# Performance work log

Measured on AMD Instinct MI355X. Metric: run time of the kernel, lower is better.

The kernel has to match this reference:

```python
import jax, jax.numpy as jnp
import numpy as np

B, C, H, N, K = 512, 256, 1024, 500000, 5

_PARAM_DIMS = [("w_in", C, H), ("w_h1", H, H), ("w_s2", H, H), ("w_s3", H, H),
               ("w_h2", H, H), ("w_s1o", H, H), ("w_s2o", H, H), ("w_h3", H, H),
               ("w_mu", H, C), ("w_s", H, C)]


def setup_inputs() -> dict:
    key = jax.random.key(0)
    inp = {}
    k_codes, k_book, k_params = jax.random.split(key, 3)
    inp["codes"] = jax.random.normal(k_codes, (B, C), dtype=jnp.float32)
    inp["codebook"] = jax.random.normal(k_book, (N, C), dtype=jnp.float32)
    ks = jax.random.split(k_params, len(_PARAM_DIMS))
    for (name, fin, fout), k in zip(_PARAM_DIMS, ks):
        k1, k2 = jax.random.split(k)
        s = 1.0 / np.sqrt(fin)
        inp[name] = jax.random.uniform(k1, (fout, fin), minval=-s, maxval=s, dtype=jnp.float32)
        inp["b" + name[1:]] = jax.random.uniform(k2, (fout,), minval=-s, maxval=s, dtype=jnp.float32)
    return inp


def _linear(x, w, b):
    # torch nn.Linear: x @ W^T + b, W is [out, in]
    return x @ w.T + b


def _encode(prev, w_in, b_in, w_h1, b_h1, w_s2, b_s2, w_s3, b_s3,
            w_h2, b_h2, w_s1o, b_s1o, w_s2o, b_s2o, w_h3, b_h3,
            w_mu, b_mu, w_s, b_s):
    i = jnp.tanh(_linear(prev, w_in, b_in))
    h1 = jnp.tanh(_linear(i, w_h1, b_h1))
    s2 = jnp.tanh(_linear(h1, w_s2, b_s2))
    s3 = jnp.tanh(_linear(h1, w_s3, b_s3))
    h2 = jnp.tanh(_linear(h1 + s2, w_h2, b_h2))
    o1 = jnp.tanh(_linear(h1, w_s1o, b_s1o))
    o2 = jnp.tanh(_linear(h2, w_s2o, b_s2o))
    o3 = jnp.tanh(_linear(h2 + s3, w_h3, b_h3))
    out = o1 + o2 + o3
    return _linear(out, w_mu, b_mu), _linear(out, w_s, b_s)


def reference(codes, codebook, w_in, b_in, w_h1, b_h1, w_s2, b_s2, w_s3, b_s3,
              w_h2, b_h2, w_s1o, b_s1o, w_s2o, b_s2o, w_h3, b_h3,
              w_mu, b_mu, w_s, b_s):
    # flat k-NN search: squared L2 dists via the matmul expansion
    codes2 = jnp.sum(codebook * codebook, axis=1)                      # [N]
    dists = (-2.0 * (codes @ codebook.T)
             + jnp.sum(codes * codes, axis=1, keepdims=True)
             + codes2[None, :])                                        # [B, N]
    neg_d, nbrs = jax.lax.top_k(-dists, K)                             # smallest K
    # eval mode: chosen_neighbor_index = 0 -> nearest neighbor
    prev = codebook[nbrs[:, 0]]                                        # [B, C]
    mu, logstd = _encode(prev, w_in, b_in, w_h1, b_h1, w_s2, b_s2, w_s3, b_s3,
                         w_h2, b_h2, w_s1o, b_s1o, w_s2o, b_s2o, w_h3, b_h3,
                         w_mu, b_mu, w_s, b_s)
    return (mu, logstd)
```

## Files before the change

kernel.cpp:

```cpp
#include <hip/hip_runtime.h>
#include <math.h>

#define QTOT   512
#define CDIM   256
#define HDIM   1024
#define NROWS  500000
#define NB     128
#define NTILES ((NROWS + NB - 1) / NB)
#define LDB    264
#define DELTA  2.0f

typedef short bf16x8 __attribute__((ext_vector_type(8)));
typedef float f32x4  __attribute__((ext_vector_type(4)));

__device__ __forceinline__ unsigned short bf16_rne(float f) {
  unsigned u = __float_as_uint(f);
  u += 0x7FFFu + ((u >> 16) & 1u);
  return (unsigned short)(u >> 16);
}
__device__ __forceinline__ unsigned bfp2(float a, float b) {
  return (unsigned)bf16_rne(a) | ((unsigned)bf16_rne(b) << 16);
}

__global__ void k_prep(const float* __restrict__ codes, unsigned short* __restrict__ a0s) {
  int q = blockIdx.x, k = threadIdx.x;
  float v = -2.0f * codes[q * CDIM + k];
  int qb = q >> 7, row = q & 127, m = row >> 4, l15 = row & 15;
  int ks = k >> 5, kin = k & 31, quad = kin >> 3, off = kin & 7;
  int lane = quad * 16 + l15;
  a0s[(((qb * 8 + m) * 8 + ks) * 64 + lane) * 8 + off] = bf16_rne(v);
}

__global__ __launch_bounds__(256, 2) void k_coarse(
    const unsigned short* __restrict__ a0s,
    const float* __restrict__ cb,
    float* __restrict__ tileMin)
{
  __shared__ __align__(16) unsigned short Bsh[128 * 256];
  __shared__ float c2sh[128];
  __shared__ float redf[512 * 2];

  const int tid  = threadIdx.x;
  const int lane = tid & 63;
  const int w    = tid >> 6;
  const int quad = lane >> 4;
  const int l15  = lane & 15;

  const int nt = blockIdx.x;
  const int n0 = nt * NB;

  const int wq = (w >> 1) * 64;
  const int wn = (w & 1) * 64;

#pragma unroll 8
  for (int j = 0; j < 32; ++j) {
    int f = j * 256 + tid;
    int row = f >> 6;
    int c4  = f & 63;
    int n   = n0 + row;
    float4 v = make_float4(0.f, 0.f, 0.f, 0.f);
    if (n < NROWS) v = *(const float4*)(cb + (size_t)n * CDIM + c4 * 4);
    float sq = v.x * v.x + v.y * v.y + v.z * v.z + v.w * v.w;
    uint2 p; p.x = bfp2(v.x, v.y); p.y = bfp2(v.z, v.w);
    int chunk = (c4 >> 1) ^ (row & 7);
    *(uint2*)((char*)Bsh + row * 512 + chunk * 16 + (c4 & 1) * 8) = p;
#pragma unroll
    for (int s = 32; s; s >>= 1) sq += __shfl_xor(sq, s);
    if (lane == 0) c2sh[row] = (n < NROWS) ? sq : 1e30f;
  }
  __syncthreads();

  float cadd[4];
#pragma unroll
  for (int j2 = 0; j2 < 4; ++j2) cadd[j2] = c2sh[wn + j2 * 16 + l15];

  for (int qb = 0; qb < 4; ++qb) {
    bf16x8 afr[4][8];
    {
      const int mg0 = (w >> 1) * 4;
      const unsigned short* base = a0s + (size_t)(qb * 8 + mg0) * 8 * 64 * 8 + lane * 8;
#pragma unroll
      for (int m = 0; m < 4; ++m)
#pragma unroll
        for (int ks = 0; ks < 8; ++ks)
          afr[m][ks] = *(const bf16x8*)(base + (m * 8 + ks) * 64 * 8);
    }

    f32x4 acc[4][4];
#pragma unroll
    for (int m = 0; m < 4; ++m)
#pragma unroll
      for (int j2 = 0; j2 < 4; ++j2) acc[m][j2] = (f32x4){0.f, 0.f, 0.f, 0.f};

#pragma unroll
    for (int ks = 0; ks < 8; ++ks) {
      bf16x8 b[4];
      const int cbase = ks * 4 + quad;
#pragma unroll
      for (int j2 = 0; j2 < 4; ++j2) {
        const int row = wn + j2 * 16 + l15;
        b[j2] = *(const bf16x8*)((const char*)Bsh + row * 512 + ((cbase ^ (row & 7)) << 4));
      }
#pragma unroll
      for (int m = 0; m < 4; ++m)
#pragma unroll
        for (int j2 = 0; j2 < 4; ++j2)
          acc[m][j2] = __builtin_amdgcn_mfma_f32_16x16x32_bf16(afr[m][ks], b[j2], acc[m][j2], 0, 0, 0);
    }

#pragma unroll
    for (int m = 0; m < 4; ++m) {
#pragma unroll
      for (int r = 0; r < 4; ++r) {
        float kk = 1e30f;
#pragma unroll
        for (int j2 = 0; j2 < 4; ++j2) kk = fminf(kk, acc[m][j2][r] + cadd[j2]);
#pragma unroll
        for (int s = 1; s < 16; s <<= 1) kk = fminf(kk, __shfl_xor(kk, s));
        if (l15 == 0) redf[(qb * 128 + wq + m * 16 + quad * 4 + r) * 2 + (w & 1)] = kk;
      }
    }
  }
  __syncthreads();

#pragma unroll
  for (int qq = 0; qq < 2; ++qq) {
    int q = qq * 256 + tid;
    tileMin[(size_t)q * NTILES + nt] = fminf(redf[q * 2], redf[q * 2 + 1]);
  }
}

__global__ __launch_bounds__(256) void k_refine(
    const float* __restrict__ codes, const float* __restrict__ cb,
    const float* __restrict__ tileMin, float* __restrict__ prev)
{
#define LCAP 96
  __shared__ float csh[256];
  __shared__ float red[256];
  __shared__ int   list[LCAP];
  __shared__ int   cnt;
  __shared__ double rd[256];
  __shared__ int    rn[256];

  const int q = blockIdx.x;
  const int tid = threadIdx.x;
  csh[tid] = codes[q * CDIM + tid];
  if (tid == 0) cnt = 0;
  const float* tm = tileMin + (size_t)q * NTILES;
  float lm = 1e30f;
  for (int t = tid; t < NTILES; t += 256) lm = fminf(lm, tm[t]);
  red[tid] = lm;
  __syncthreads();
  for (int s = 128; s; s >>= 1) {
    if (tid < s) red[tid] = fminf(red[tid], red[tid + s]);
    __syncthreads();
  }
  const float thresh = red[0] + DELTA;
  for (int t = tid; t < NTILES; t += 256)
    if (tm[t] <= thresh) { int p = atomicAdd(&cnt, 1); if (p < LCAP) list[p] = t; }
  __syncthreads();
  const int nl = min(cnt, LCAP);

  double bestK = 1e300; int bestN = 0x7FFFFFFF;
  for (int li = 0; li < nl; ++li) {
    const int t = list[li];
    const int row = tid >> 1, half = tid & 1;
    const int n = t * NB + row;
    if (n < NROWS) {
      const float* r = cb + (size_t)n * CDIM;
      double dot = 0.0, sq = 0.0;
      for (int u = half * 32; u < half * 32 + 32; ++u) {
        float4 cv = *(const float4*)(r + u * 4);
        dot += (double)cv.x * csh[u*4+0] + (double)cv.y * csh[u*4+1]
             + (double)cv.z * csh[u*4+2] + (double)cv.w * csh[u*4+3];
        sq  += (double)cv.x * cv.x + (double)cv.y * cv.y
             + (double)cv.z * cv.z + (double)cv.w * cv.w;
      }
      dot += __shfl_xor(dot, 1);
      sq  += __shfl_xor(sq, 1);
      double key = sq - 2.0 * dot;
      if (key < bestK || (key == bestK && n < bestN)) { bestK = key; bestN = n; }
    }
  }
  rd[tid] = bestK; rn[tid] = bestN;
  __syncthreads();
  for (int s = 128; s; s >>= 1) {
    if (tid < s) {
      if (rd[tid + s] < rd[tid] || (rd[tid + s] == rd[tid] && rn[tid + s] < rn[tid])) {
        rd[tid] = rd[tid + s]; rn[tid] = rn[tid + s];
      }
    }
    __syncthreads();
  }
  const int nstar = rn[0];
  prev[(size_t)q * CDIM + tid] = cb[(size_t)nstar * CDIM + tid];
}

struct Job {
  const float* A1; const float* A2; const float* A3;
  const float* W;  const float* bias; float* out;
};

__global__ __launch_bounds__(256) void k_gemm(
    Job j0, Job j1, Job j2, int Kdim, int Ntot, int do_tanh)
{
  __shared__ unsigned short Ash[128 * LDB];
  __shared__ unsigned short Wsh[64 * LDB];
  __shared__ float bsh[64];

  const Job jb = (blockIdx.z == 0) ? j0 : ((blockIdx.z == 1) ? j1 : j2);
  const float* __restrict__ A1 = jb.A1;
  const float* __restrict__ A2 = jb.A2;
  const float* __restrict__ A3 = jb.A3;
  const float* __restrict__ W  = jb.W;

  const int tid  = threadIdx.x;
  const int lane = tid & 63;
  const int w    = tid >> 6;
  const int quad = lane >> 4;
  const int l15  = lane & 15;
  const int q0   = blockIdx.x * 128;
  const int n0   = blockIdx.y * 64;

  if (tid < 64) bsh[tid] = jb.bias[n0 + tid];

  f32x4 acc[2][4];
#pragma unroll
  for (int m = 0; m < 2; ++m)
#pragma unroll
    for (int j = 0; j < 4; ++j) acc[m][j] = (f32x4){0.f, 0.f, 0.f, 0.f};

  for (int kc = 0; kc < Kdim; kc += 256) {
    __syncthreads();
#pragma unroll 4
    for (int it = 0; it < 32; ++it) {
      int i = it * 256 + tid;
      int row = i >> 6, c4 = i & 63;
      size_t gi = (size_t)(q0 + row) * Kdim + kc + c4 * 4;
      float4 v = *(const float4*)(A1 + gi);
      if (A2) { float4 u = *(const float4*)(A2 + gi); v.x += u.x; v.y += u.y; v.z += u.z; v.w += u.w; }
      if (A3) { float4 u = *(const float4*)(A3 + gi); v.x += u.x; v.y += u.y; v.z += u.z; v.w += u.w; }
      uint2 p; p.x = bfp2(v.x, v.y); p.y = bfp2(v.z, v.w);
      *(uint2*)&Ash[row * LDB + c4 * 4] = p;
    }
#pragma unroll 4
    for (int it = 0; it < 16; ++it) {
      int i = it * 256 + tid;
      int row = i >> 6, c4 = i & 63;
      size_t gi = (size_t)(n0 + row) * Kdim + kc + c4 * 4;
      float4 v = *(const float4*)(W + gi);
      uint2 p; p.x = bfp2(v.x, v.y); p.y = bfp2(v.z, v.w);
      *(uint2*)&Wsh[row * LDB + c4 * 4] = p;
    }
    __syncthreads();
#pragma unroll
    for (int ks = 0; ks < 8; ++ks) {
      const int kb = ks * 32 + quad * 8;
      bf16x8 a[2], b[4];
#pragma unroll
      for (int m = 0; m < 2; ++m)
        a[m] = *(const bf16x8*)&Ash[(w * 32 + m * 16 + l15) * LDB + kb];
#pragma unroll
      for (int j = 0; j < 4; ++j)
        b[j] = *(const bf16x8*)&Wsh[(j * 16 + l15) * LDB + kb];
#pragma unroll
      for (int m = 0; m < 2; ++m)
#pragma unroll
        for (int j = 0; j < 4; ++j)
          acc[m][j] = __builtin_amdgcn_mfma_f32_16x16x32_bf16(a[m], b[j], acc[m][j], 0, 0, 0);
    }
  }

#pragma unroll
  for (int m = 0; m < 2; ++m)
#pragma unroll
    for (int j = 0; j < 4; ++j)
#pragma unroll
      for (int r = 0; r < 4; ++r) {
        int q = q0 + w * 32 + m * 16 + quad * 4 + r;
        int n = j * 16 + l15;
        float v = acc[m][j][r] + bsh[n];
        if (do_tanh) v = tanhf(v);
        jb.out[(size_t)q * Ntot + n0 + n] = v;
      }
}

extern "C" void kernel_launch(void* const* d_in, const int* in_sizes, int n_in,
                              void* d_out, int out_size, void* d_ws, size_t ws_size,
                              hipStream_t stream) {
  const float* codes = (const float*)d_in[0];
  const float* cb    = (const float*)d_in[1];
  const float* w_in  = (const float*)d_in[2];
  const float* b_in  = (const float*)d_in[3];
  const float* w_h1  = (const float*)d_in[4];
  const float* b_h1  = (const float*)d_in[5];
  const float* w_s2  = (const float*)d_in[6];
  const float* b_s2  = (const float*)d_in[7];
  const float* w_s3  = (const float*)d_in[8];
  const float* b_s3  = (const float*)d_in[9];
  const float* w_h2  = (const float*)d_in[10];
  const float* b_h2  = (const float*)d_in[11];
  const float* w_s1o = (const float*)d_in[12];
  const float* b_s1o = (const float*)d_in[13];
  const float* w_s2o = (const float*)d_in[14];
  const float* b_s2o = (const float*)d_in[15];
  const float* w_h3  = (const float*)d_in[16];
  const float* b_h3  = (const float*)d_in[17];
  const float* w_mu  = (const float*)d_in[18];
  const float* b_mu  = (const float*)d_in[19];
  const float* w_s   = (const float*)d_in[20];
  const float* b_s   = (const float*)d_in[21];
  float* out = (float*)d_out;

  char* ws = (char*)d_ws;
  unsigned short* a0s = (unsigned short*)ws;
  float* tileMin = (float*)(ws + 262144);
  float* prev    = (float*)(ws + 262144 + 8001536);
  float* acts    = (float*)(ws + 262144 + 8001536 + 524288);
  const int ACT = 512 * 1024;
  float* act_i  = acts + 0 * ACT;
  float* act_h1 = acts + 1 * ACT;
  float* act_s2 = acts + 2 * ACT;
  float* act_s3 = acts + 3 * ACT;
  float* act_h2 = acts + 4 * ACT;
  float* act_o1 = acts + 5 * ACT;
  float* act_o2 = acts + 6 * ACT;
  float* act_o3 = acts + 7 * ACT;

  hipLaunchKernelGGL(k_prep,   dim3(512),    dim3(256), 0, stream, codes, a0s);
  hipLaunchKernelGGL(k_coarse, dim3(NTILES), dim3(256), 0, stream, a0s, cb, tileMin);
  hipLaunchKernelGGL(k_refine, dim3(512),    dim3(256), 0, stream, codes, cb, tileMin, prev);

  const float* NUL = nullptr;
  Job in_j  = { prev,   NUL,    NUL,    w_in,  b_in,  act_i  };
  Job h1_j  = { act_i,  NUL,    NUL,    w_h1,  b_h1,  act_h1 };
  Job s2_j  = { act_h1, NUL,    NUL,    w_s2,  b_s2,  act_s2 };
  Job s3_j  = { act_h1, NUL,    NUL,    w_s3,  b_s3,  act_s3 };
  Job o1_j  = { act_h1, NUL,    NUL,    w_s1o, b_s1o, act_o1 };
  Job h2_j  = { act_h1, act_s2, NUL,    w_h2,  b_h2,  act_h2 };
  Job o2_j  = { act_h2, NUL,    NUL,    w_s2o, b_s2o, act_o2 };
  Job o3_j  = { act_h2, act_s3, NUL,    w_h3,  b_h3,  act_o3 };
  Job mu_j  = { act_o1, act_o2, act_o3, w_mu,  b_mu,  out            };
  Job ls_j  = { act_o1, act_o2, act_o3, w_s,   b_s,   out + 131072   };

  hipLaunchKernelGGL(k_gemm, dim3(4, 16, 1), dim3(256), 0, stream, in_j, in_j, in_j, 256,  1024, 1);
  hipLaunchKernelGGL(k_gemm, dim3(4, 16, 1), dim3(256), 0, stream, h1_j, h1_j, h1_j, 1024, 1024, 1);
  hipLaunchKernelGGL(k_gemm, dim3(4, 16, 3), dim3(256), 0, stream, s2_j, s3_j, o1_j, 1024, 1024, 1);
  hipLaunchKernelGGL(k_gemm, dim3(4, 16, 1), dim3(256), 0, stream, h2_j, h2_j, h2_j, 1024, 1024, 1);
  hipLaunchKernelGGL(k_gemm, dim3(4, 16, 2), dim3(256), 0, stream, o2_j, o3_j, o3_j, 1024, 1024, 1);
  hipLaunchKernelGGL(k_gemm, dim3(4, 4, 2),  dim3(256), 0, stream, mu_j, ls_j, ls_j, 1024, 256,  0);
}
```

Baseline: 1.376 ms.

## Pre-convert codebook to bf16 in two L2-sized chunks before coarse kNN pass

Adds a conversion kernel that turns codebook rows into swizzled bf16 together with their squared norms. The coarse distance kernel is split into two chunks, each run right after its own conversion, so the converted data is likely still in cache when read. The coarse kernel now fills shared memory with direct global-to-LDS loads, streams A fragments with a 3-deep prefetch instead of holding all of them in registers, and uses DPP for its min reductions. The cost is an extra read and write of the codebook plus two more launches, and the old path is kept as a fallback when the workspace is too small.

```diff
diff --git a/kernel.cpp b/kernel.cpp
--- a/kernel.cpp
+++ b/kernel.cpp
@@ -7,11 +7,18 @@
 #define NROWS  500000
 #define NB     128
 #define NTILES ((NROWS + NB - 1) / NB)
+#define NPADR  (NTILES * NB)
 #define LDB    264
 #define DELTA  2.0f
 
+#define C0_T   1954
+#define C1_T   (NTILES - C0_T)
+#define C0_R   (C0_T * NB)
+#define C1_R   (C1_T * NB)
+
 typedef short bf16x8 __attribute__((ext_vector_type(8)));
 typedef float f32x4  __attribute__((ext_vector_type(4)));
+typedef unsigned int u32;
 
 __device__ __forceinline__ unsigned short bf16_rne(float f) {
   unsigned u = __float_as_uint(f);
@@ -21,6 +28,18 @@
 __device__ __forceinline__ unsigned bfp2(float a, float b) {
   return (unsigned)bf16_rne(a) | ((unsigned)bf16_rne(b) << 16);
 }
+
+__device__ __forceinline__ void gld16(const void* g, void* l) {
+  __builtin_amdgcn_global_load_lds((const __attribute__((address_space(1))) u32*)g,
+                                   (__attribute__((address_space(3))) u32*)l, 16, 0, 0);
+}
+
+#define FMIN_DPP(x, ctrl) do { \
+    int _t = __builtin_amdgcn_update_dpp(__float_as_int(x), __float_as_int(x), (ctrl), 0xF, 0xF, false); \
+    x = fminf(x, __int_as_float(_t)); } while (0)
+#define FADD_DPP(x, ctrl) do { \
+    int _t = __builtin_amdgcn_update_dpp(__float_as_int(x), __float_as_int(x), (ctrl), 0xF, 0xF, false); \
+    x += __int_as_float(_t); } while (0)
 
 __global__ void k_prep(const float* __restrict__ codes, unsigned short* __restrict__ a0s) {
   int q = blockIdx.x, k = threadIdx.x;
@@ -31,7 +50,129 @@
   a0s[(((qb * 8 + m) * 8 + ks) * 64 + lane) * 8 + off] = bf16_rne(v);
 }
 
+__global__ __launch_bounds__(256) void k_conv(
+    const float* __restrict__ cb, unsigned short* __restrict__ cbh,
+    float* __restrict__ c2, int row0, int nrows)
+{
+  const int lane = threadIdx.x & 63;
+  const int wid  = (blockIdx.x * 256 + threadIdx.x) >> 6;
+  const int nw   = (gridDim.x * 256) >> 6;
+  for (int r = wid; r < nrows; r += nw) {
+    const int gr = row0 + r;
+    float4 v = make_float4(0.f, 0.f, 0.f, 0.f);
+    if (gr < NROWS) v = *(const float4*)(cb + (size_t)gr * CDIM + lane * 4);
+    float sq = v.x * v.x + v.y * v.y + v.z * v.z + v.w * v.w;
+    FADD_DPP(sq, 0xB1);
+    FADD_DPP(sq, 0x4E);
+    FADD_DPP(sq, 0x124);
+    FADD_DPP(sq, 0x128);
+    sq += __shfl_xor(sq, 16);
+    sq += __shfl_xor(sq, 32);
+    uint2 p; p.x = bfp2(v.x, v.y); p.y = bfp2(v.z, v.w);
+    *(uint2*)((char*)cbh + (size_t)r * 512 + lane * 8) = p;
+    if (lane == 0) c2[r] = (gr < NROWS) ? sq : 1e30f;
+  }
+}
+
 __global__ __launch_bounds__(256, 2) void k_coarse(
+    const unsigned short* __restrict__ a0s,
+    const unsigned short* __restrict__ cbh,
+    const float* __restrict__ c2arr,
+    float* __restrict__ tileMin, int nt0)
+{
+  __shared__ __align__(16) unsigned short Bsh[128 * 256];
+  __shared__ float c2sh[128];
+  __shared__ float redf[512 * 2];
+
+  const int tid  = threadIdx.x;
+  const int lane = tid & 63;
+  const int w    = tid >> 6;
+  const int quad = lane >> 4;
+  const int l15  = lane & 15;
+
+  const int ntl  = blockIdx.x;
+  const int ntg  = nt0 + ntl;
+
+  const int wq = (w >> 1) * 64;
+  const int wn = (w & 1) * 64;
+
+  {
+    const char* tbase = (const char*)cbh + (size_t)ntl * 65536;
+#pragma unroll
+    for (int i2 = 0; i2 < 16; ++i2) {
+      const int i   = w * 16 + i2;
+      const int row = 2 * i + (lane >> 5);
+      const int cS  = lane & 31;
+      gld16(tbase + (size_t)row * 512 + ((cS ^ (row & 7)) << 4),
+            (char*)Bsh + i * 1024);
+    }
+  }
+  if (tid < 128) c2sh[tid] = c2arr[ntl * NB + tid];
+  __syncthreads();
+
+  float cadd[4];
+#pragma unroll
+  for (int j2 = 0; j2 < 4; ++j2) cadd[j2] = c2sh[wn + j2 * 16 + l15];
+
+  for (int qb = 0; qb < 4; ++qb) {
+    const unsigned short* abase = a0s + (size_t)(qb * 8 + (w >> 1) * 4) * 4096 + lane * 8;
+
+    f32x4 acc[4][4];
+#pragma unroll
+    for (int m = 0; m < 4; ++m)
+#pragma unroll
+      for (int j2 = 0; j2 < 4; ++j2) acc[m][j2] = (f32x4){0.f, 0.f, 0.f, 0.f};
+
+    bf16x8 apf[3][4];
+#pragma unroll
+    for (int m = 0; m < 4; ++m) apf[0][m] = *(const bf16x8*)(abase + (m * 8 + 0) * 512);
+#pragma unroll
+    for (int m = 0; m < 4; ++m) apf[1][m] = *(const bf16x8*)(abase + (m * 8 + 1) * 512);
+
+#pragma unroll
+    for (int ks = 0; ks < 8; ++ks) {
+      if (ks + 2 < 8) {
+#pragma unroll
+        for (int m = 0; m < 4; ++m)
+          apf[(ks + 2) % 3][m] = *(const bf16x8*)(abase + (m * 8 + ks + 2) * 512);
+      }
+      bf16x8 b[4];
+#pragma unroll
+      for (int j2 = 0; j2 < 4; ++j2) {
+        const int row = wn + j2 * 16 + l15;
+        b[j2] = *(const bf16x8*)((const char*)Bsh + row * 512 + (((ks * 4 + quad) ^ (row & 7)) << 4));
+      }
+#pragma unroll
+      for (int m = 0; m < 4; ++m)
+#pragma unroll
+        for (int j2 = 0; j2 < 4; ++j2)
+          acc[m][j2] = __builtin_amdgcn_mfma_f32_16x16x32_bf16(apf[ks % 3][m], b[j2], acc[m][j2], 0, 0, 0);
+    }
+
+#pragma unroll
+    for (int m = 0; m < 4; ++m) {
+#pragma unroll
+      for (int r = 0; r < 4; ++r) {
+        float kk = fminf(fminf(acc[m][0][r] + cadd[0], acc[m][1][r] + cadd[1]),
+                         fminf(acc[m][2][r] + cadd[2], acc[m][3][r] + cadd[3]));
+        FMIN_DPP(kk, 0xB1);
+        FMIN_DPP(kk, 0x4E);
+        FMIN_DPP(kk, 0x124);
+        FMIN_DPP(kk, 0x128);
+        if (l15 == 0) redf[(qb * 128 + wq + m * 16 + quad * 4 + r) * 2 + (w & 1)] = kk;
+      }
+    }
+  }
+  __syncthreads();
+
+#pragma unroll
+  for (int qq = 0; qq < 2; ++qq) {
+    int q = qq * 256 + tid;
+    tileMin[(size_t)q * NTILES + ntg] = fminf(redf[q * 2], redf[q * 2 + 1]);
+  }
+}
+
+__global__ __launch_bounds__(256, 2) void k_coarse_fb(
     const unsigned short* __restrict__ a0s,
     const float* __restrict__ cb,
     float* __restrict__ tileMin)
@@ -85,13 +226,11 @@
         for (int ks = 0; ks < 8; ++ks)
           afr[m][ks] = *(const bf16x8*)(base + (m * 8 + ks) * 64 * 8);
     }
-
     f32x4 acc[4][4];
 #pragma unroll
     for (int m = 0; m < 4; ++m)
 #pragma unroll
       for (int j2 = 0; j2 < 4; ++j2) acc[m][j2] = (f32x4){0.f, 0.f, 0.f, 0.f};
-
 #pragma unroll
     for (int ks = 0; ks < 8; ++ks) {
       bf16x8 b[4];
@@ -107,7 +246,6 @@
         for (int j2 = 0; j2 < 4; ++j2)
           acc[m][j2] = __builtin_amdgcn_mfma_f32_16x16x32_bf16(afr[m][ks], b[j2], acc[m][j2], 0, 0, 0);
     }
-
 #pragma unroll
     for (int m = 0; m < 4; ++m) {
 #pragma unroll
@@ -327,9 +465,25 @@
   float* act_o2 = acts + 6 * ACT;
   float* act_o3 = acts + 7 * ACT;
 
-  hipLaunchKernelGGL(k_prep,   dim3(512),    dim3(256), 0, stream, codes, a0s);
-  hipLaunchKernelGGL(k_coarse, dim3(NTILES), dim3(256), 0, stream, a0s, cb, tileMin);
-  hipLaunchKernelGGL(k_refine, dim3(512),    dim3(256), 0, stream, codes, cb, tileMin, prev);
+  const size_t CBH_OFF = 262144 + 8001536 + 524288 + 16777216;
+  const size_t CBH_SZ  = (size_t)C0_R * 512;
+  const size_t C2_OFF  = CBH_OFF + CBH_SZ;
+  const size_t NEED    = C2_OFF + (size_t)C0_R * 4;
+  unsigned short* cbh = (unsigned short*)(ws + CBH_OFF);
+  float* c2buf        = (float*)(ws + C2_OFF);
+
+  hipLaunchKernelGGL(k_prep, dim3(512), dim3(256), 0, stream, codes, a0s);
+
+  if (ws_size >= NEED) {
+    hipLaunchKernelGGL(k_conv,   dim3(2048), dim3(256), 0, stream, cb, cbh, c2buf, 0, C0_R);
+    hipLaunchKernelGGL(k_coarse, dim3(C0_T), dim3(256), 0, stream, a0s, cbh, c2buf, tileMin, 0);
+    hipLaunchKernelGGL(k_conv,   dim3(2048), dim3(256), 0, stream, cb, cbh, c2buf, C0_R, C1_R);
+    hipLaunchKernelGGL(k_coarse, dim3(C1_T), dim3(256), 0, stream, a0s, cbh, c2buf, tileMin, C0_T);
+  } else {
+    hipLaunchKernelGGL(k_coarse_fb, dim3(NTILES), dim3(256), 0, stream, a0s, cb, tileMin);
+  }
+
+  hipLaunchKernelGGL(k_refine, dim3(512), dim3(256), 0, stream, codes, cb, tileMin, prev);
 
   const float* NUL = nullptr;
   Job in_j  = { prev,   NUL,    NUL,    w_in,  b_in,  act_i  };
```

Measured after the change: 1.332 ms. -3.2%, faster.
